# Optimization experiments

Measured on AMD Instinct MI355X. Metric: run time of the kernel, lower is better.

Reference implementation:

```python
import jax, jax.numpy as jnp
import numpy as np

H = 768
F = 3072
NH = 12
EPS = 1e-5


def _layer_norm(x, g, b):
    mu = jnp.mean(x, axis=-1, keepdims=True)
    var = jnp.mean(jnp.square(x - mu), axis=-1, keepdims=True)
    return (x - mu) * jax.lax.rsqrt(var + EPS) * g + b


def setup_inputs() -> dict:
    key = jax.random.key(0)
    ks = jax.random.split(key, 16)
    s = 0.02
    d = {
        'x': jax.random.normal(ks[0], (2, 2048, H), jnp.float32),
        'Wq': jax.random.normal(ks[1], (H, H), jnp.float32) * s,
        'bq': jnp.zeros((H,), jnp.float32),
        'Wk': jax.random.normal(ks[2], (H, H), jnp.float32) * s,
        'bk': jnp.zeros((H,), jnp.float32),
        'Wv': jax.random.normal(ks[3], (H, H), jnp.float32) * s,
        'bv': jnp.zeros((H,), jnp.float32),
        'Wa1': jax.random.normal(ks[4], (H, H), jnp.float32) * s,
        'ba1': jnp.zeros((H,), jnp.float32),
        'g1': jnp.ones((H,), jnp.float32),
        'be1': jnp.zeros((H,), jnp.float32),
        'W1': jax.random.normal(ks[5], (H, F), jnp.float32) * s,
        'b1': jnp.zeros((F,), jnp.float32),
        'W2': jax.random.normal(ks[6], (F, H), jnp.float32) * s,
        'b2': jnp.zeros((H,), jnp.float32),
        'Wa2': jax.random.normal(ks[7], (H, H), jnp.float32) * s,
        'ba2': jnp.zeros((H,), jnp.float32),
        'g2': jnp.ones((H,), jnp.float32),
        'be2': jnp.zeros((H,), jnp.float32),
    }
    return d


def reference(x, Wq, bq, Wk, bk, Wv, bv, Wa1, ba1, g1, be1, W1, b1, W2, b2, Wa2, ba2, g2, be2):
    B, S, _ = x.shape
    Dh = H // NH
    # multi-head attention (naive: explicit scores + softmax)
    q = (x @ Wq + bq).reshape(B, S, NH, Dh)
    k = (x @ Wk + bk).reshape(B, S, NH, Dh)
    v = (x @ Wv + bv).reshape(B, S, NH, Dh)
    scores = jnp.einsum('bqhd,bkhd->bhqk', q, k) / jnp.sqrt(jnp.float32(Dh))
    att = jax.nn.softmax(scores, axis=-1)
    ctx = jnp.einsum('bhqk,bkhd->bqhd', att, v).reshape(B, S, H)
    # add_norm_1: Linear -> LayerNorm, then residual added AFTER LN (as in source)
    an1 = _layer_norm(ctx @ Wa1 + ba1, g1, be1) + x
    # feed-forward with exact GELU (torch nn.GELU default)
    ff = jax.nn.gelu(an1 @ W1 + b1, approximate=False) @ W2 + b2
    # add_norm_2: Linear -> LayerNorm, residual after LN
    out = _layer_norm(ff @ Wa2 + ba2, g2, be2) + an1
    return out
```

## Files before the change

### kernel.cpp

```cpp
#include <hip/hip_runtime.h>
#include <stdint.h>
#include <stddef.h>

#define HD 768
#define FF 3072
#define NHEAD 12
#define DHEAD 64
#define SEQ 2048
#define BATCH 2
#define NTOK (SEQ*BATCH)
#define SM_SCALE 0.18033688f

typedef __attribute__((ext_vector_type(8))) __bf16 bf16x8;
typedef __attribute__((ext_vector_type(4))) float f32x4;

__device__ __forceinline__ unsigned short f2bf(float f) {
  unsigned int u = __builtin_bit_cast(unsigned int, f);
  u += 0x7fffu + ((u >> 16) & 1u);
  return (unsigned short)(u >> 16);
}

__device__ __forceinline__ void gl16(const unsigned short* g, unsigned short* l) {
  __builtin_amdgcn_global_load_lds(
      (const __attribute__((address_space(1))) void*)g,
      (__attribute__((address_space(3))) void*)l,
      16, 0, 0);
}


__global__ void k_cvt(const float* __restrict__ in, unsigned short* __restrict__ out, int n4,
                      const float* __restrict__ bq, const float* __restrict__ bk,
                      const float* __restrict__ bv, float* __restrict__ biasqkv) {
  if (blockIdx.x < 9) {
    int idx = blockIdx.x * 256 + threadIdx.x;
    if (idx < 3*HD) {
      float v = idx < HD ? bq[idx] : idx < 2*HD ? bk[idx-HD] : bv[idx-2*HD];
      biasqkv[idx] = v;
    }
  }
  int i = blockIdx.x * blockDim.x + threadIdx.x;
  int stride = gridDim.x * blockDim.x;
  for (; i < n4; i += stride) {
    float4 v = reinterpret_cast<const float4*>(in)[i];
    ushort4 o;
    o.x = f2bf(v.x); o.y = f2bf(v.y); o.z = f2bf(v.z); o.w = f2bf(v.w);
    reinterpret_cast<ushort4*>(out)[i] = o;
  }
}

__global__ void k_prep_w(const float* __restrict__ Wq, const float* __restrict__ Wk,
                         const float* __restrict__ Wv, const float* __restrict__ Wa1,
                         const float* __restrict__ W1, const float* __restrict__ W2,
                         const float* __restrict__ Wa2,
                         unsigned short* __restrict__ WqkvT, unsigned short* __restrict__ Wa1T,
                         unsigned short* __restrict__ W1T, unsigned short* __restrict__ W2T,
                         unsigned short* __restrict__ Wa2T) {
  __shared__ float tile[32][33];
  int t = blockIdx.x;
  const float* in; unsigned short* out; int K, N;
  if (t < 2304)      { int seg = t / 576; t -= seg * 576; K = HD; N = HD;
                       in  = seg==0 ? Wq : seg==1 ? Wk : seg==2 ? Wv : Wa1;
                       out = seg<3 ? WqkvT + seg*HD*HD : Wa1T; }
  else if (t < 4608) { t -= 2304; in = W1;  out = W1T;  K = HD; N = FF; }
  else if (t < 6912) { t -= 4608; in = W2;  out = W2T;  K = FF; N = HD; }
  else               { t -= 6912; in = Wa2; out = Wa2T; K = HD; N = HD; }
  int nt = N / 32;
  int nb = (t % nt) * 32, kb = (t / nt) * 32;
  int tx = threadIdx.x, ty = threadIdx.y;
  for (int i = ty; i < 32; i += 8)
    tile[i][tx] = in[(size_t)(kb + i) * N + nb + tx];
  __syncthreads();
  for (int i = ty; i < 32; i += 8)
    out[(size_t)(nb + i) * K + kb + tx] = f2bf(tile[tx][i]);
}

__global__ void k_vtrans(const unsigned short* __restrict__ qkv, unsigned short* __restrict__ vt) {
  __shared__ unsigned short tile[32][33];
  int st = blockIdx.x * 32;
  int ct = blockIdx.y * 32;
  int b = blockIdx.z;
  int tx = threadIdx.x, ty = threadIdx.y;
  for (int i = ty; i < 32; i += 8)
    tile[i][tx] = qkv[(size_t)(b*SEQ + st + i) * 2304 + 2*HD + ct + tx];
  __syncthreads();
  for (int i = ty; i < 32; i += 8) {
    int vcol = ct + i;
    int p = st + tx;
    int k64 = p & 63;
    int news = (p & ~63) + ((k64 >> 2) & 3) * 16 + (k64 >> 4) * 4 + (k64 & 3);
    vt[((size_t)(b*NHEAD + (vcol >> 6)) * DHEAD + (vcol & 63)) * SEQ + news] = tile[tx][i];
  }
}


#define BN 128
#define BK 32

template<int MODE, int TBM>
__global__ __launch_bounds__(256, 3)
void k_gemm(const unsigned short* __restrict__ A, const unsigned short* __restrict__ Bt,
            const float* __restrict__ bias, void* __restrict__ Cout,
            int M, int N, int K) {
  constexpr int MR = TBM / 32;
  constexpr int AI = TBM / 64;
  __shared__ unsigned short As[TBM*BK];
  __shared__ unsigned short Bs[BN*BK];
  int tid = threadIdx.x;
  int bm = blockIdx.x * TBM;
  int bn = blockIdx.y * BN;
  int wave = tid >> 6, lane = tid & 63;
  int wm = wave >> 1, wn = wave & 1;
  int wr = wm * (TBM/2);
  int wc = wn * 64;
  int fr = lane & 15;
  int kb = (lane >> 4) * 8;

  f32x4 acc[MR][4];
#pragma unroll
  for (int m = 0; m < MR; ++m)
#pragma unroll
    for (int n = 0; n < 4; ++n) acc[m][n] = (f32x4){0.f,0.f,0.f,0.f};

  int scol = (lane & 3) * 8;
  int srowA = AI*16*wave + (lane >> 2);
  int srowB = 32*wave + (lane >> 2);
  const unsigned short* ag = A + (size_t)(bm + srowA) * K + scol;
  const unsigned short* bg = Bt + (size_t)(bn + srowB) * K + scol;
  unsigned short* asl = As + AI*16*wave*BK;
  unsigned short* bsl = Bs + 32*wave*BK;

  for (int k0 = 0; k0 < K; k0 += BK) {
#pragma unroll
    for (int i = 0; i < AI; ++i)
      gl16(ag + (size_t)(16*i)*K + k0, asl + 16*i*BK);
#pragma unroll
    for (int i = 0; i < 2; ++i)
      gl16(bg + (size_t)(16*i)*K + k0, bsl + 16*i*BK);
    __syncthreads();

    bf16x8 af[MR], bfv[4];
#pragma unroll
    for (int m = 0; m < MR; ++m)
      af[m] = __builtin_bit_cast(bf16x8, *reinterpret_cast<const uint4*>(&As[(wr + m*16 + fr)*BK + kb]));
#pragma unroll
    for (int n = 0; n < 4; ++n)
      bfv[n] = __builtin_bit_cast(bf16x8, *reinterpret_cast<const uint4*>(&Bs[(wc + n*16 + fr)*BK + kb]));
#pragma unroll
    for (int m = 0; m < MR; ++m)
#pragma unroll
      for (int n = 0; n < 4; ++n)
        acc[m][n] = __builtin_amdgcn_mfma_f32_16x16x32_bf16(af[m], bfv[n], acc[m][n], 0, 0, 0);
    __syncthreads();
  }

  int crow0 = (lane >> 4) * 4;
  int ccol = lane & 15;
#pragma unroll
  for (int m = 0; m < MR; ++m) {
#pragma unroll
    for (int n = 0; n < 4; ++n) {
      int gcol = bn + wc + n*16 + ccol;
      float bv_ = bias[gcol];
#pragma unroll
      for (int r = 0; r < 4; ++r) {
        int grow = bm + wr + m*16 + crow0 + r;
        float v = acc[m][n][r] + bv_;
        if (MODE == 2) v = 0.5f * v * (1.0f + erff(v * 0.70710678118f));
        if (MODE == 3 && gcol < HD) v *= SM_SCALE;
        if (MODE == 0) reinterpret_cast<float*>(Cout)[(size_t)grow * N + gcol] = v;
        else           reinterpret_cast<unsigned short*>(Cout)[(size_t)grow * N + gcol] = f2bf(v);
      }
    }
  }
}


#define KVB 64
#define KP 72

__global__ __launch_bounds__(256, 3)
void k_attn_mfma(const unsigned short* __restrict__ qkv,
                 const unsigned short* __restrict__ vt,
                 unsigned short* __restrict__ ctx) {
  __shared__ unsigned short Ks[KVB][KP];
  __shared__ unsigned short Vt[DHEAD][KP];
  __shared__ f32x4 Mg[2][9][64];

  int tid = threadIdx.x;
  int wv = tid >> 6, lane = tid & 63;
  int lo = lane & 15, hi = lane >> 4;
  int qh = wv & 1;
  int kh = wv >> 1;

  int lin = blockIdx.x + 32*(blockIdx.y + NHEAD*blockIdx.z);
  int nl = (lin & 7) * 96 + (lin >> 3);
  int qb = nl & 31;
  int rest = nl >> 5;
  int h = rest % NHEAD;
  int b = rest / NHEAD;
  int q0 = qb * 64;

  const unsigned short* qpA = qkv + (size_t)(b*SEQ + q0 + qh*32 + lo) * 2304 + h*DHEAD + hi*8;
  const unsigned short* qpB = qpA + (size_t)16 * 2304;
  bf16x8 qfA0 = __builtin_bit_cast(bf16x8, *reinterpret_cast<const uint4*>(qpA));
  bf16x8 qfA1 = __builtin_bit_cast(bf16x8, *reinterpret_cast<const uint4*>(qpA + 32));
  bf16x8 qfB0 = __builtin_bit_cast(bf16x8, *reinterpret_cast<const uint4*>(qpB));
  bf16x8 qfB1 = __builtin_bit_cast(bf16x8, *reinterpret_cast<const uint4*>(qpB + 32));

  f32x4 poA[4], poB[4];
#pragma unroll
  for (int dt = 0; dt < 4; ++dt) { poA[dt] = (f32x4){0.f,0.f,0.f,0.f}; poB[dt] = (f32x4){0.f,0.f,0.f,0.f}; }
  float lrA = 0.f, lrB = 0.f;

  int sr = tid >> 2, scg = (tid & 3) * 16;
  const unsigned short* kgl = qkv + (size_t)(b*SEQ)*2304 + HD + h*DHEAD;
  const unsigned short* vgl = vt + ((size_t)(b*NHEAD + h)) * DHEAD * SEQ;

  for (int t0 = 0; t0 < SEQ; t0 += KVB) {
    const unsigned short* kp = kgl + (size_t)(t0 + sr)*2304 + scg;
    const unsigned short* vp = vgl + (size_t)sr*SEQ + t0 + scg;
    uint4 ku0 = *reinterpret_cast<const uint4*>(kp);
    uint4 ku1 = *reinterpret_cast<const uint4*>(kp + 8);
    uint4 vu0 = *reinterpret_cast<const uint4*>(vp);
    uint4 vu1 = *reinterpret_cast<const uint4*>(vp + 8);
    __syncthreads();
    *reinterpret_cast<uint4*>(&Ks[sr][scg])     = ku0;
    *reinterpret_cast<uint4*>(&Ks[sr][scg + 8]) = ku1;
    *reinterpret_cast<uint4*>(&Vt[sr][scg])     = vu0;
    *reinterpret_cast<uint4*>(&Vt[sr][scg + 8]) = vu1;
    __syncthreads();

    f32x4 sA[2], sB[2];
#pragma unroll
    for (int kg = 0; kg < 2; ++kg) {
      int krow = kh*32 + kg*16 + lo;
      bf16x8 a0 = __builtin_bit_cast(bf16x8, *reinterpret_cast<const uint4*>(&Ks[krow][hi*8]));
      bf16x8 a1 = __builtin_bit_cast(bf16x8, *reinterpret_cast<const uint4*>(&Ks[krow][32 + hi*8]));
      f32x4 s = (f32x4){0.f,0.f,0.f,0.f};
      s = __builtin_amdgcn_mfma_f32_16x16x32_bf16(a0, qfA0, s, 0, 0, 0);
      s = __builtin_amdgcn_mfma_f32_16x16x32_bf16(a1, qfA1, s, 0, 0, 0);
      sA[kg] = s;
      s = (f32x4){0.f,0.f,0.f,0.f};
      s = __builtin_amdgcn_mfma_f32_16x16x32_bf16(a0, qfB0, s, 0, 0, 0);
      s = __builtin_amdgcn_mfma_f32_16x16x32_bf16(a1, qfB1, s, 0, 0, 0);
      sB[kg] = s;
    }

    float tsA = 0.f, tsB = 0.f;
    unsigned int pwA[4], pwB[4];
#pragma unroll
    for (int kg = 0; kg < 2; ++kg) {
      float a0 = exp2f(sA[kg][0]), a1 = exp2f(sA[kg][1]);
      float a2 = exp2f(sA[kg][2]), a3 = exp2f(sA[kg][3]);
      tsA += a0 + a1 + a2 + a3;
      asm("v_cvt_pk_bf16_f32 %0, %1, %2" : "=v"(pwA[kg*2])   : "v"(a0), "v"(a1));
      asm("v_cvt_pk_bf16_f32 %0, %1, %2" : "=v"(pwA[kg*2+1]) : "v"(a2), "v"(a3));
      float b0 = exp2f(sB[kg][0]), b1 = exp2f(sB[kg][1]);
      float b2 = exp2f(sB[kg][2]), b3 = exp2f(sB[kg][3]);
      tsB += b0 + b1 + b2 + b3;
      asm("v_cvt_pk_bf16_f32 %0, %1, %2" : "=v"(pwB[kg*2])   : "v"(b0), "v"(b1));
      asm("v_cvt_pk_bf16_f32 %0, %1, %2" : "=v"(pwB[kg*2+1]) : "v"(b2), "v"(b3));
    }
    tsA += __shfl_xor(tsA, 16); tsA += __shfl_xor(tsA, 32); lrA += tsA;
    tsB += __shfl_xor(tsB, 16); tsB += __shfl_xor(tsB, 32); lrB += tsB;

    uint4 uA; uA.x = pwA[0]; uA.y = pwA[1]; uA.z = pwA[2]; uA.w = pwA[3];
    uint4 uB; uB.x = pwB[0]; uB.y = pwB[1]; uB.z = pwB[2]; uB.w = pwB[3];
    bf16x8 paA = __builtin_bit_cast(bf16x8, uA);
    bf16x8 paB = __builtin_bit_cast(bf16x8, uB);

#pragma unroll
    for (int dt = 0; dt < 4; ++dt) {
      int col = dt*16 + lo;
      bf16x8 vv = __builtin_bit_cast(bf16x8, *reinterpret_cast<const uint4*>(&Vt[col][hi*16 + kh*8]));
      poA[dt] = __builtin_amdgcn_mfma_f32_16x16x32_bf16(paA, vv, poA[dt], 0, 0, 0);
      poB[dt] = __builtin_amdgcn_mfma_f32_16x16x32_bf16(paB, vv, poB[dt], 0, 0, 0);
    }
  }

  if (kh == 1) {
#pragma unroll
    for (int dt = 0; dt < 4; ++dt) {
      Mg[qh][dt][lane] = poA[dt];
      Mg[qh][4 + dt][lane] = poB[dt];
    }
    Mg[qh][8][lane] = (f32x4){lrA, lrB, 0.f, 0.f};
  }
  __syncthreads();
  if (kh == 0) {
#pragma unroll
    for (int dt = 0; dt < 4; ++dt) {
      f32x4 mA = Mg[qh][dt][lane], mB = Mg[qh][4 + dt][lane];
      poA[dt][0] += mA[0]; poA[dt][1] += mA[1]; poA[dt][2] += mA[2]; poA[dt][3] += mA[3];
      poB[dt][0] += mB[0]; poB[dt][1] += mB[1]; poB[dt][2] += mB[2]; poB[dt][3] += mB[3];
    }
    f32x4 lm = Mg[qh][8][lane];
    lrA += lm[0]; lrB += lm[1];

    unsigned short* op = ctx + (size_t)(b*SEQ + q0 + qh*32) * HD + h*DHEAD;
#pragma unroll
    for (int r = 0; r < 4; ++r) {
      float LA = __shfl(lrA, hi*4 + r);
      float LB = __shfl(lrB, hi*4 + r);
      float liA = (LA > 0.f) ? 1.0f / LA : 0.f;
      float liB = (LB > 0.f) ? 1.0f / LB : 0.f;
      int row = hi*4 + r;
#pragma unroll
      for (int dt = 0; dt < 4; ++dt) {
        op[(size_t)row*HD + dt*16 + lo]        = f2bf(poA[dt][r] * liA);
        op[(size_t)(16 + row)*HD + dt*16 + lo] = f2bf(poB[dt][r] * liB);
      }
    }
  }
}

template<int WRITE_BF16>
__global__ __launch_bounds__(256, 4)
void k_ln(const float* __restrict__ xin, const float* __restrict__ resid,
          const float* __restrict__ g, const float* __restrict__ be,
          float* __restrict__ outf, unsigned short* __restrict__ outb) {
  int wave = threadIdx.x >> 6, lane = threadIdx.x & 63;
  int row = blockIdx.x * 4 + wave;
  const float4* xp = reinterpret_cast<const float4*>(xin + (size_t)row * HD);
  const float4* rp = reinterpret_cast<const float4*>(resid + (size_t)row * HD);
  const float4* gp = reinterpret_cast<const float4*>(g);
  const float4* bp = reinterpret_cast<const float4*>(be);
  float4 v[3];
  float sum = 0.f, sq = 0.f;
#pragma unroll
  for (int i = 0; i < 3; ++i) {
    v[i] = xp[lane + 64*i];
    sum += v[i].x + v[i].y + v[i].z + v[i].w;
    sq  += v[i].x*v[i].x + v[i].y*v[i].y + v[i].z*v[i].z + v[i].w*v[i].w;
  }
#pragma unroll
  for (int m = 1; m < 64; m <<= 1) { sum += __shfl_xor(sum, m); sq += __shfl_xor(sq, m); }
  float mean = sum * (1.0f/768.0f);
  float var = sq * (1.0f/768.0f) - mean*mean;
  float rstd = rsqrtf(var + 1e-5f);
#pragma unroll
  for (int i = 0; i < 3; ++i) {
    float4 gg = gp[lane + 64*i], bb = bp[lane + 64*i], rr = rp[lane + 64*i];
    float4 o;
    o.x = (v[i].x - mean)*rstd*gg.x + bb.x + rr.x;
    o.y = (v[i].y - mean)*rstd*gg.y + bb.y + rr.y;
    o.z = (v[i].z - mean)*rstd*gg.z + bb.z + rr.z;
    o.w = (v[i].w - mean)*rstd*gg.w + bb.w + rr.w;
    reinterpret_cast<float4*>(outf + (size_t)row * HD)[lane + 64*i] = o;
    if (WRITE_BF16) {
      ushort4 ob;
      ob.x = f2bf(o.x); ob.y = f2bf(o.y); ob.z = f2bf(o.z); ob.w = f2bf(o.w);
      reinterpret_cast<ushort4*>(outb + (size_t)row * HD)[lane + 64*i] = ob;
    }
  }
}


extern "C" void kernel_launch(void* const* d_in, const int* in_sizes, int n_in,
                              void* d_out, int out_size, void* d_ws, size_t ws_size,
                              hipStream_t stream) {
  const float* x   = (const float*)d_in[0];
  const float* Wq  = (const float*)d_in[1];
  const float* bq  = (const float*)d_in[2];
  const float* Wk  = (const float*)d_in[3];
  const float* bk  = (const float*)d_in[4];
  const float* Wv  = (const float*)d_in[5];
  const float* bv  = (const float*)d_in[6];
  const float* Wa1 = (const float*)d_in[7];
  const float* ba1 = (const float*)d_in[8];
  const float* g1  = (const float*)d_in[9];
  const float* be1 = (const float*)d_in[10];
  const float* W1  = (const float*)d_in[11];
  const float* b1  = (const float*)d_in[12];
  const float* W2  = (const float*)d_in[13];
  const float* b2  = (const float*)d_in[14];
  const float* Wa2 = (const float*)d_in[15];
  const float* ba2 = (const float*)d_in[16];
  const float* g2  = (const float*)d_in[17];
  const float* be2 = (const float*)d_in[18];

  char* ws = (char*)d_ws;
  size_t off = 0;
  auto alloc = [&](size_t bytes) -> void* {
    void* p = ws + off;
    off += (bytes + 255) & ~(size_t)255;
    return p;
  };
  unsigned short* xb    = (unsigned short*)alloc((size_t)NTOK*HD*2);
  unsigned short* WqkvT = (unsigned short*)alloc((size_t)3*HD*HD*2);
  unsigned short* Wa1T  = (unsigned short*)alloc((size_t)HD*HD*2);
  unsigned short* W1T   = (unsigned short*)alloc((size_t)FF*HD*2);
  unsigned short* W2T   = (unsigned short*)alloc((size_t)HD*FF*2);
  unsigned short* Wa2T  = (unsigned short*)alloc((size_t)HD*HD*2);
  float*          biasqkv = (float*)alloc((size_t)3*HD*4);
  unsigned short* qkvb  = (unsigned short*)alloc((size_t)NTOK*3*HD*2);
  unsigned short* vtb   = (unsigned short*)alloc((size_t)NTOK*HD*2);
  unsigned short* ctxb  = (unsigned short*)alloc((size_t)NTOK*HD*2);
  float*          a1    = (float*)alloc((size_t)NTOK*HD*4);
  float*          an1f  = (float*)alloc((size_t)NTOK*HD*4);
  unsigned short* an1b  = (unsigned short*)alloc((size_t)NTOK*HD*2);
  unsigned short* h1g   = (unsigned short*)alloc((size_t)NTOK*FF*2);
  unsigned short* f2b   = (unsigned short*)alloc((size_t)NTOK*HD*2);
  float*          a2    = (float*)alloc((size_t)NTOK*HD*4);
  (void)ws_size; (void)in_sizes; (void)n_in; (void)out_size;

  dim3 t32x8(32, 8);
  k_cvt<<<2048, 256, 0, stream>>>(x, xb, NTOK*HD/4, bq, bk, bv, biasqkv);
  k_prep_w<<<7488, t32x8, 0, stream>>>(Wq, Wk, Wv, Wa1, W1, W2, Wa2,
                                       WqkvT, Wa1T, W1T, W2T, Wa2T);

  k_gemm<3,128><<<dim3(NTOK/128, 2304/BN), 256, 0, stream>>>(xb, WqkvT, biasqkv, qkvb, NTOK, 3*HD, HD);
  k_vtrans<<<dim3(SEQ/32, HD/32, BATCH), t32x8, 0, stream>>>(qkvb, vtb);
  k_attn_mfma<<<dim3(SEQ/64, NHEAD, BATCH), 256, 0, stream>>>(qkvb, vtb, ctxb);
  k_gemm<0,64><<<dim3(NTOK/64, HD/BN), 256, 0, stream>>>(ctxb, Wa1T, ba1, a1, NTOK, HD, HD);
  k_ln<1><<<NTOK/4, 256, 0, stream>>>(a1, x, g1, be1, an1f, an1b);
  k_gemm<2,128><<<dim3(NTOK/128, FF/BN), 256, 0, stream>>>(an1b, W1T, b1, h1g, NTOK, FF, HD);
  k_gemm<1,64><<<dim3(NTOK/64, HD/BN), 256, 0, stream>>>(h1g, W2T, b2, f2b, NTOK, HD, FF);
  k_gemm<0,64><<<dim3(NTOK/64, HD/BN), 256, 0, stream>>>(f2b, Wa2T, ba2, a2, NTOK, HD, HD);
  k_ln<0><<<NTOK/4, 256, 0, stream>>>(a2, an1f, g2, be2, (float*)d_out, nullptr);
}
```

Baseline: 226.4 us.

## Double GEMM K-tile to 64 with XOR-swizzled LDS and merge prep kernels

Raises the GEMM K-tile from 32 to 64 so each block issues two MFMAs per fragment pair between barriers, halving the number of sync/load rounds. The LDS layout uses an XOR swizzle on 16-byte chunks, applied consistently on the async global-to-LDS loads and the fragment reads, to avoid bank conflicts. Separately, the activation-conversion and weight-transpose prep kernels are merged into one launch to save a kernel launch. The larger tile doubles LDS use per block, which may reduce occupancy.

```diff
diff --git a/kernel.cpp b/kernel.cpp
--- a/kernel.cpp
+++ b/kernel.cpp
@@ -27,36 +27,38 @@
       16, 0, 0);
 }
 
-
-__global__ void k_cvt(const float* __restrict__ in, unsigned short* __restrict__ out, int n4,
-                      const float* __restrict__ bq, const float* __restrict__ bk,
-                      const float* __restrict__ bv, float* __restrict__ biasqkv) {
-  if (blockIdx.x < 9) {
-    int idx = blockIdx.x * 256 + threadIdx.x;
-    if (idx < 3*HD) {
-      float v = idx < HD ? bq[idx] : idx < 2*HD ? bk[idx-HD] : bv[idx-2*HD];
-      biasqkv[idx] = v;
-    }
-  }
-  int i = blockIdx.x * blockDim.x + threadIdx.x;
-  int stride = gridDim.x * blockDim.x;
-  for (; i < n4; i += stride) {
-    float4 v = reinterpret_cast<const float4*>(in)[i];
-    ushort4 o;
-    o.x = f2bf(v.x); o.y = f2bf(v.y); o.z = f2bf(v.z); o.w = f2bf(v.w);
-    reinterpret_cast<ushort4*>(out)[i] = o;
-  }
-}
-
-__global__ void k_prep_w(const float* __restrict__ Wq, const float* __restrict__ Wk,
-                         const float* __restrict__ Wv, const float* __restrict__ Wa1,
-                         const float* __restrict__ W1, const float* __restrict__ W2,
-                         const float* __restrict__ Wa2,
-                         unsigned short* __restrict__ WqkvT, unsigned short* __restrict__ Wa1T,
-                         unsigned short* __restrict__ W1T, unsigned short* __restrict__ W2T,
-                         unsigned short* __restrict__ Wa2T) {
+__global__ void k_prep(const float* __restrict__ Wq, const float* __restrict__ Wk,
+                       const float* __restrict__ Wv, const float* __restrict__ Wa1,
+                       const float* __restrict__ W1, const float* __restrict__ W2,
+                       const float* __restrict__ Wa2,
+                       unsigned short* __restrict__ WqkvT, unsigned short* __restrict__ Wa1T,
+                       unsigned short* __restrict__ W1T, unsigned short* __restrict__ W2T,
+                       unsigned short* __restrict__ Wa2T,
+                       const float* __restrict__ x, unsigned short* __restrict__ xb, int n4,
+                       const float* __restrict__ bq, const float* __restrict__ bk,
+                       const float* __restrict__ bv, float* __restrict__ biasqkv) {
+  int t = blockIdx.x;
+  int tid = threadIdx.x;
+  if (t >= 7488) {
+    int tb = t - 7488;
+    if (tb < 9) {
+      int idx = tb * 256 + tid;
+      if (idx < 3*HD) {
+        float v = idx < HD ? bq[idx] : idx < 2*HD ? bk[idx-HD] : bv[idx-2*HD];
+        biasqkv[idx] = v;
+      }
+    }
+    int i = tb * 256 + tid;
+    int stride = 2048 * 256;
+    for (; i < n4; i += stride) {
+      float4 v = reinterpret_cast<const float4*>(x)[i];
+      ushort4 o;
+      o.x = f2bf(v.x); o.y = f2bf(v.y); o.z = f2bf(v.z); o.w = f2bf(v.w);
+      reinterpret_cast<ushort4*>(xb)[i] = o;
+    }
+    return;
+  }
   __shared__ float tile[32][33];
-  int t = blockIdx.x;
   const float* in; unsigned short* out; int K, N;
   if (t < 2304)      { int seg = t / 576; t -= seg * 576; K = HD; N = HD;
                        in  = seg==0 ? Wq : seg==1 ? Wk : seg==2 ? Wv : Wa1;
@@ -66,7 +68,7 @@
   else               { t -= 6912; in = Wa2; out = Wa2T; K = HD; N = HD; }
   int nt = N / 32;
   int nb = (t % nt) * 32, kb = (t / nt) * 32;
-  int tx = threadIdx.x, ty = threadIdx.y;
+  int tx = tid & 31, ty = tid >> 5;
   for (int i = ty; i < 32; i += 8)
     tile[i][tx] = in[(size_t)(kb + i) * N + nb + tx];
   __syncthreads();
@@ -94,7 +96,7 @@
 
 
 #define BN 128
-#define BK 32
+#define BK 64
 
 template<int MODE, int TBM>
 __global__ __launch_bounds__(256, 3)
@@ -102,7 +104,7 @@
             const float* __restrict__ bias, void* __restrict__ Cout,
             int M, int N, int K) {
   constexpr int MR = TBM / 32;
-  constexpr int AI = TBM / 64;
+  constexpr int AI = TBM / 32;
   __shared__ unsigned short As[TBM*BK];
   __shared__ unsigned short Bs[BN*BK];
   int tid = threadIdx.x;
@@ -113,7 +115,7 @@
   int wr = wm * (TBM/2);
   int wc = wn * 64;
   int fr = lane & 15;
-  int kb = (lane >> 4) * 8;
+  int hi = lane >> 4;
 
   f32x4 acc[MR][4];
 #pragma unroll
@@ -121,35 +123,48 @@
 #pragma unroll
     for (int n = 0; n < 4; ++n) acc[m][n] = (f32x4){0.f,0.f,0.f,0.f};
 
-  int scol = (lane & 3) * 8;
-  int srowA = AI*16*wave + (lane >> 2);
-  int srowB = 32*wave + (lane >> 2);
-  const unsigned short* ag = A + (size_t)(bm + srowA) * K + scol;
-  const unsigned short* bg = Bt + (size_t)(bn + srowB) * K + scol;
-  unsigned short* asl = As + AI*16*wave*BK;
+  int g8 = lane >> 3;
+  int cc = (lane & 7) ^ g8;
+  int arow = (TBM/4)*wave + g8;
+  int brow = 32*wave + g8;
+  const unsigned short* ag = A + (size_t)(bm + arow) * K + cc*8;
+  const unsigned short* bg = Bt + (size_t)(bn + brow) * K + cc*8;
+  unsigned short* asl = As + (TBM/4)*wave*BK;
   unsigned short* bsl = Bs + 32*wave*BK;
 
   for (int k0 = 0; k0 < K; k0 += BK) {
 #pragma unroll
     for (int i = 0; i < AI; ++i)
-      gl16(ag + (size_t)(16*i)*K + k0, asl + 16*i*BK);
-#pragma unroll
-    for (int i = 0; i < 2; ++i)
-      gl16(bg + (size_t)(16*i)*K + k0, bsl + 16*i*BK);
+      gl16(ag + (size_t)(8*i)*K + k0, asl + (8*i)*BK);
+#pragma unroll
+    for (int i = 0; i < 4; ++i)
+      gl16(bg + (size_t)(8*i)*K + k0, bsl + (8*i)*BK);
     __syncthreads();
 
-    bf16x8 af[MR], bfv[4];
+    bf16x8 af[MR][2], bf[4][2];
+#pragma unroll
+    for (int m = 0; m < MR; ++m) {
+      int R = wr + m*16 + fr, sw = R & 7;
+#pragma unroll
+      for (int h2 = 0; h2 < 2; ++h2)
+        af[m][h2] = __builtin_bit_cast(bf16x8,
+          *reinterpret_cast<const uint4*>(&As[R*BK + ((hi + h2*4) ^ sw)*8]));
+    }
+#pragma unroll
+    for (int n = 0; n < 4; ++n) {
+      int R = wc + n*16 + fr, sw = R & 7;
+#pragma unroll
+      for (int h2 = 0; h2 < 2; ++h2)
+        bf[n][h2] = __builtin_bit_cast(bf16x8,
+          *reinterpret_cast<const uint4*>(&Bs[R*BK + ((hi + h2*4) ^ sw)*8]));
+    }
 #pragma unroll
     for (int m = 0; m < MR; ++m)
-      af[m] = __builtin_bit_cast(bf16x8, *reinterpret_cast<const uint4*>(&As[(wr + m*16 + fr)*BK + kb]));
-#pragma unroll
-    for (int n = 0; n < 4; ++n)
-      bfv[n] = __builtin_bit_cast(bf16x8, *reinterpret_cast<const uint4*>(&Bs[(wc + n*16 + fr)*BK + kb]));
-#pragma unroll
-    for (int m = 0; m < MR; ++m)
-#pragma unroll
-      for (int n = 0; n < 4; ++n)
-        acc[m][n] = __builtin_amdgcn_mfma_f32_16x16x32_bf16(af[m], bfv[n], acc[m][n], 0, 0, 0);
+#pragma unroll
+      for (int n = 0; n < 4; ++n) {
+        acc[m][n] = __builtin_amdgcn_mfma_f32_16x16x32_bf16(af[m][0], bf[n][0], acc[m][n], 0, 0, 0);
+        acc[m][n] = __builtin_amdgcn_mfma_f32_16x16x32_bf16(af[m][1], bf[n][1], acc[m][n], 0, 0, 0);
+      }
     __syncthreads();
   }
 
@@ -405,9 +420,9 @@
   (void)ws_size; (void)in_sizes; (void)n_in; (void)out_size;
 
   dim3 t32x8(32, 8);
-  k_cvt<<<2048, 256, 0, stream>>>(x, xb, NTOK*HD/4, bq, bk, bv, biasqkv);
-  k_prep_w<<<7488, t32x8, 0, stream>>>(Wq, Wk, Wv, Wa1, W1, W2, Wa2,
-                                       WqkvT, Wa1T, W1T, W2T, Wa2T);
+  k_prep<<<9536, 256, 0, stream>>>(Wq, Wk, Wv, Wa1, W1, W2, Wa2,
+                                   WqkvT, Wa1T, W1T, W2T, Wa2T,
+                                   x, xb, NTOK*HD/4, bq, bk, bv, biasqkv);
 
   k_gemm<3,128><<<dim3(NTOK/128, 2304/BN), 256, 0, stream>>>(xb, WqkvT, biasqkv, qkvb, NTOK, 3*HD, HD);
   k_vtrans<<<dim3(SEQ/32, HD/32, BATCH), t32x8, 0, stream>>>(qkvb, vtb);
```

Result: faster. 198.4 us (-12.4%).
